# Optimization experiments

Measured on AMD Instinct MI355X. Metric: run time of the kernel, lower is better.

## Reference

```python
import jax, jax.numpy as jnp
import numpy as np

NUM_HEADS = 16
WINDOW = 16  # hard-coded in module; half-window = 8


def sliding_mask(seq_len):
    # mask[i, j] = 0 if j in [i - W//2, i + W//2], else -inf  (additive)
    i = jnp.arange(seq_len)[:, None]
    j = jnp.arange(seq_len)[None, :]
    return jnp.where(jnp.abs(i - j) <= WINDOW // 2, 0.0, -jnp.inf).astype(jnp.float32)


def setup_inputs() -> dict:
    key = jax.random.key(0)
    k1, k2, k3 = jax.random.split(key, 3)
    B, S, D = 2, 2048, 1024
    scale = 1.0 / np.sqrt(D)
    return {
        "input_embeddings": jax.random.normal(k1, (B, S, D), dtype=jnp.float32),
        "token_ids": jax.random.randint(k2, (B, S), 0, 32000, dtype=jnp.int64),
        # nn.MultiheadAttention params: packed in_proj [3D, D] + bias, out_proj [D, D] + bias
        "w_qkv": jax.random.normal(jax.random.fold_in(k3, 0), (3 * D, D), dtype=jnp.float32) * scale,
        "b_qkv": jnp.zeros((3 * D,), dtype=jnp.float32),
        "w_out": jax.random.normal(jax.random.fold_in(k3, 1), (D, D), dtype=jnp.float32) * scale,
        "b_out": jnp.zeros((D,), dtype=jnp.float32),
    }


def reference(input_embeddings, token_ids, w_qkv, b_qkv, w_out, b_out):
    B, S, D = input_embeddings.shape
    H = NUM_HEADS
    hd = D // H
    # packed QKV projection (torch in_proj): [B, S, 3D]
    qkv = input_embeddings @ w_qkv.T + b_qkv
    q, k, v = jnp.split(qkv, 3, axis=-1)
    # [B, H, S, hd]
    q = q.reshape(B, S, H, hd).transpose(0, 2, 1, 3)
    k = k.reshape(B, S, H, hd).transpose(0, 2, 1, 3)
    v = v.reshape(B, S, H, hd).transpose(0, 2, 1, 3)
    scores = jnp.einsum("bhqd,bhkd->bhqk", q, k) / jnp.sqrt(jnp.asarray(hd, q.dtype))
    scores = scores + sliding_mask(S)  # broadcast additive [S, S] mask
    attn = jax.nn.softmax(scores, axis=-1)
    ctx = jnp.einsum("bhqk,bhkd->bhqd", attn, v)
    ctx = ctx.transpose(0, 2, 1, 3).reshape(B, S, D)
    return ctx @ w_out.T + b_out
```

## Files before the change

kernel.cpp:

```cpp
#include <hip/hip_runtime.h>
#include <stdint.h>


typedef __bf16 bf16_t;
typedef bf16_t bf16x8 __attribute__((ext_vector_type(8)));
typedef unsigned short u16x8 __attribute__((ext_vector_type(8)));
typedef float f32x4 __attribute__((ext_vector_type(4)));

#define GLD16(g, l)                                                        \
  __builtin_amdgcn_global_load_lds(                                        \
      (const __attribute__((address_space(1))) void*)(g),                  \
      (__attribute__((address_space(3))) void*)(l), 16, 0, 0)

__device__ __forceinline__ unsigned short f2bf(float f) {
  unsigned int u = __float_as_uint(f);
  u += 0x7FFFu + ((u >> 16) & 1u);
  return (unsigned short)(u >> 16);
}

__device__ __forceinline__ bf16x8 ld16(const unsigned short* p) {
  return __builtin_bit_cast(bf16x8, *reinterpret_cast<const u16x8*>(p));
}

__global__ void cvt_all(const float* __restrict__ x, const float* __restrict__ wq,
                        const float* __restrict__ wo, unsigned short* __restrict__ xb,
                        unsigned short* __restrict__ wqb,
                        unsigned short* __restrict__ wob) {
  const int N0 = 1048576, N1 = 786432, N2 = 262144;
  for (int i = blockIdx.x * blockDim.x + threadIdx.x; i < N0 + N1 + N2;
       i += gridDim.x * blockDim.x) {
    const float4* src;
    unsigned short* dst;
    int j;
    if (i < N0) { src = (const float4*)x; dst = xb; j = i; }
    else if (i < N0 + N1) { src = (const float4*)wq; dst = wqb; j = i - N0; }
    else { src = (const float4*)wo; dst = wob; j = i - N0 - N1; }
    const float4 f = src[j];
    ushort4 o;
    o.x = f2bf(f.x); o.y = f2bf(f.y); o.z = f2bf(f.z); o.w = f2bf(f.w);
    reinterpret_cast<ushort4*>(dst)[j] = o;
  }
}

template <int EPI>
__global__ __launch_bounds__(256, 2) void gemm_bt(
    const unsigned short* __restrict__ A,
    const unsigned short* __restrict__ Bt,
    const float* __restrict__ bias,
    unsigned short* __restrict__ Cq, unsigned short* __restrict__ Ck,
    unsigned short* __restrict__ Cv, float* __restrict__ Cp, int M, int N,
    int K) {
  __shared__ unsigned short sA[2][8192];
  __shared__ unsigned short sB[2][8192];

  const int tid = threadIdx.x;
  const int wave = tid >> 6;
  const int lane = tid & 63;
  const int m0 = blockIdx.x * 128;
  const int n0 = blockIdx.y * 128;
  const int wr = wave >> 1;
  const int wc = wave & 1;

  f32x4 acc[4][4] = {};

  const int srow = (wave << 3) + (lane >> 3);
  const int sslot = ((lane & 7) ^ (lane >> 3)) << 3;
  const unsigned short* Ag = A + (size_t)(m0 + srow) * K + sslot;
  const unsigned short* Bg = Bt + (size_t)(n0 + srow) * K + sslot;
  const int wdst = wave * 512;

  const int T = K >> 6;

  auto stage = [&](int t, int b) {
#pragma unroll
    for (int r = 0; r < 4; ++r) {
      GLD16(Ag + (size_t)(r * 32) * K + t * 64, &sA[b][r * 2048 + wdst]);
      GLD16(Bg + (size_t)(r * 32) * K + t * 64, &sB[b][r * 2048 + wdst]);
    }
  };

  stage(0, 0);
  stage(1, 1);

  const int kg = lane >> 4;
  const int l7 = lane & 7;
  const int arr = wr * 64 + (lane & 15);
  const int brr = wc * 64 + (lane & 15);

  for (int t = 0; t < T; ++t) {
    if (t < T - 1)
      asm volatile("s_waitcnt vmcnt(8)" ::: "memory");
    else
      asm volatile("s_waitcnt vmcnt(0)" ::: "memory");
    __builtin_amdgcn_s_barrier();

    const int b = t & 1;
    const unsigned short* sAb = sA[b];
    const unsigned short* sBb = sB[b];
    bf16x8 af[2][4], bfr[2][4];
#pragma unroll
    for (int st = 0; st < 2; ++st) {
#pragma unroll
      for (int f = 0; f < 4; ++f) {
        const int se = ((st << 2) | kg) ^ l7;
        af[st][f] = ld16(&sAb[(arr + f * 16) * 64 + (se << 3)]);
        bfr[st][f] = ld16(&sBb[(brr + f * 16) * 64 + (se << 3)]);
      }
    }
    asm volatile("s_waitcnt lgkmcnt(0)" ::: "memory");
    __builtin_amdgcn_sched_barrier(0);
    __builtin_amdgcn_s_barrier();

    if (t + 2 < T) stage(t + 2, b);

#pragma unroll
    for (int st = 0; st < 2; ++st)
#pragma unroll
      for (int i = 0; i < 4; ++i)
#pragma unroll
        for (int j = 0; j < 4; ++j)
          acc[i][j] = __builtin_amdgcn_mfma_f32_16x16x32_bf16(
              af[st][i], bfr[st][j], acc[i][j], 0, 0, 0);
  }

#pragma unroll
  for (int i = 0; i < 4; ++i) {
    const int row0 = m0 + wr * 64 + i * 16 + ((lane >> 4) << 2);
#pragma unroll
    for (int j = 0; j < 4; ++j) {
      const int col = n0 + wc * 64 + j * 16 + (lane & 15);
      const float bb = bias[col];
#pragma unroll
      for (int r = 0; r < 4; ++r) {
        const int m = row0 + r;
        const float val = acc[i][j][r] + bb;
        if (EPI == 0) {
          Cp[(size_t)m * N + col] = val;
        } else {
          const int b2 = m >> 11, s = m & 2047;
          const int which = col >> 10, nn = col & 1023;
          const int h = nn >> 6, d = nn & 63;
          const int bh = (b2 << 4) + h;
          const unsigned short vb = f2bf(val);
          if (which == 0)
            Cq[((size_t)(bh * 2048 + s)) * 64 + d] = vb;
          else if (which == 1)
            Ck[((size_t)(bh * 2048 + s)) * 64 + d] = vb;
          else
            Cv[((size_t)(bh * 64 + d)) * 2048 + s] = vb;
        }
      }
    }
  }
}

__global__ __launch_bounds__(256) void attn_mfma(
    const unsigned short* __restrict__ Qb, const unsigned short* __restrict__ Kb,
    const unsigned short* __restrict__ Vt, unsigned short* __restrict__ ctx) {
  __shared__ unsigned short P[4][16][40];
  const int wave = threadIdx.x >> 6;
  const int lane = threadIdx.x & 63;
  const int gw = (blockIdx.x << 2) + wave;
  const int bh = gw >> 7;
  const int i0 = (gw & 127) << 4;
  const int qr = lane & 15;
  const int kg = lane >> 4;
  const int kc = kg << 3;

  const size_t qbase = ((size_t)(bh * 2048 + i0 + qr)) * 64;
  const bf16x8 aq0 = ld16(Qb + qbase + kc);
  const bf16x8 aq1 = ld16(Qb + qbase + 32 + kc);

  f32x4 sc0 = {0.f, 0.f, 0.f, 0.f}, sc1 = {0.f, 0.f, 0.f, 0.f};
  {
    const int ka0 = i0 - 8 + qr;
    const int ka1 = ka0 + 16;
    const int kcl0 = min(max(ka0, 0), 2047);
    const int kcl1 = min(max(ka1, 0), 2047);
    const unsigned short* K0 = Kb + ((size_t)(bh * 2048 + kcl0)) * 64;
    const unsigned short* K1 = Kb + ((size_t)(bh * 2048 + kcl1)) * 64;
    sc0 = __builtin_amdgcn_mfma_f32_16x16x32_bf16(aq0, ld16(K0 + kc), sc0, 0, 0, 0);
    sc0 = __builtin_amdgcn_mfma_f32_16x16x32_bf16(aq1, ld16(K0 + 32 + kc), sc0, 0, 0, 0);
    sc1 = __builtin_amdgcn_mfma_f32_16x16x32_bf16(aq0, ld16(K1 + kc), sc1, 0, 0, 0);
    sc1 = __builtin_amdgcn_mfma_f32_16x16x32_bf16(aq1, ld16(K1 + 32 + kc), sc1, 0, 0, 0);
  }

  unsigned short* Pw = &P[wave][0][0];
  float lsum[4];
#pragma unroll
  for (int r = 0; r < 4; ++r) {
    const int q = (kg << 2) + r;
    const int key0 = qr, key1 = 16 + qr;
    const int ka0 = i0 - 8 + key0, ka1 = i0 - 8 + key1;
    const bool v0 = (q <= key0) && (key0 <= q + 16) && (ka0 >= 0) && (ka0 < 2048);
    const bool v1 = (q <= key1) && (key1 <= q + 16) && (ka1 >= 0) && (ka1 < 2048);
    const float e0 = v0 ? __expf(sc0[r] * 0.125f) : 0.f;
    const float e1 = v1 ? __expf(sc1[r] * 0.125f) : 0.f;
    Pw[q * 40 + key0] = f2bf(e0);
    Pw[q * 40 + key1] = f2bf(e1);
    float s = e0 + e1;
#pragma unroll
    for (int off = 1; off < 16; off <<= 1) s += __shfl_xor(s, off);
    lsum[r] = s;
  }

  const bf16x8 pa = ld16(&Pw[qr * 40 + kc]);

  const int base_s = min(max(i0 - 8 + kc, 0), 2040);
  f32x4 o[4];
  const f32x4 zero = {0.f, 0.f, 0.f, 0.f};
#pragma unroll
  for (int t2 = 0; t2 < 4; ++t2) {
    const unsigned short* Vr =
        Vt + ((size_t)(bh * 64 + t2 * 16 + qr)) * 2048 + base_s;
    o[t2] = __builtin_amdgcn_mfma_f32_16x16x32_bf16(pa, ld16(Vr), zero, 0, 0, 0);
  }

  const int b = bh >> 4, h = bh & 15;
  float rinv[4];
#pragma unroll
  for (int r = 0; r < 4; ++r) rinv[r] = 1.0f / lsum[r];
#pragma unroll
  for (int t2 = 0; t2 < 4; ++t2) {
#pragma unroll
    for (int r = 0; r < 4; ++r) {
      const int q = (kg << 2) + r;
      const int d = t2 * 16 + qr;
      ctx[((size_t)(b * 2048 + i0 + q)) * 1024 + (h << 6) + d] =
          f2bf(o[t2][r] * rinv[r]);
    }
  }
}

extern "C" void kernel_launch(void* const* d_in, const int* in_sizes, int n_in,
                              void* d_out, int out_size, void* d_ws,
                              size_t ws_size, hipStream_t stream) {
  const float* x = (const float*)d_in[0];
  const float* w_qkv = (const float*)d_in[2];
  const float* b_qkv = (const float*)d_in[3];
  const float* w_out = (const float*)d_in[4];
  const float* b_out = (const float*)d_in[5];
  float* out = (float*)d_out;

  char* ws = (char*)d_ws;
  unsigned short* xb    = (unsigned short*)(ws + 0);
  unsigned short* wqkvb = (unsigned short*)(ws + 8388608);
  unsigned short* woutb = (unsigned short*)(ws + 14680064);
  unsigned short* Qb    = (unsigned short*)(ws + 16777216);
  unsigned short* Kb    = (unsigned short*)(ws + 25165824);
  unsigned short* Vt    = (unsigned short*)(ws + 33554432);
  unsigned short* ctxb  = (unsigned short*)(ws + 41943040);

  cvt_all<<<2048, 256, 0, stream>>>(x, w_qkv, w_out, xb, wqkvb, woutb);

  gemm_bt<1><<<dim3(32, 24), 256, 0, stream>>>(xb, wqkvb, b_qkv, Qb, Kb, Vt,
                                               nullptr, 4096, 3072, 1024);

  attn_mfma<<<1024, 256, 0, stream>>>(Qb, Kb, Vt, ctxb);

  gemm_bt<0><<<dim3(32, 8), 256, 0, stream>>>(ctxb, woutb, b_out, nullptr,
                                              nullptr, nullptr, out, 4096,
                                              1024, 1024);
}
```

Before: 79.73 us.

## Enlarge GEMM tiles to 256x256 with 512 threads and XCD-aware block remap

The GEMM kernel moves from 128x128 tiles with 256 threads to 256x256 tiles with 512 threads (8 waves in a 2x4 grid, each holding 8x4 MFMA accumulators). This raises arithmetic intensity per byte loaded into LDS. Block ids are remapped so consecutive ids are spread across the 8 XCDs, and the first k-half MFMAs are issued before the second half's LDS reads to overlap them. The risk is that the grid shrinks to 192 and 64 blocks, which may underfill the 256 CUs, especially for the output projection. Register pressure also rises.

```diff
diff --git a/kernel.cpp b/kernel.cpp
--- a/kernel.cpp
+++ b/kernel.cpp
@@ -43,25 +43,30 @@
 }
 
 template <int EPI>
-__global__ __launch_bounds__(256, 2) void gemm_bt(
+__global__ __launch_bounds__(512, 1) void gemm_bt(
     const unsigned short* __restrict__ A,
     const unsigned short* __restrict__ Bt,
     const float* __restrict__ bias,
     unsigned short* __restrict__ Cq, unsigned short* __restrict__ Ck,
     unsigned short* __restrict__ Cv, float* __restrict__ Cp, int M, int N,
-    int K) {
-  __shared__ unsigned short sA[2][8192];
-  __shared__ unsigned short sB[2][8192];
+    int K, int gny) {
+  __shared__ unsigned short sA[2][16384];
+  __shared__ unsigned short sB[2][16384];
 
   const int tid = threadIdx.x;
   const int wave = tid >> 6;
   const int lane = tid & 63;
-  const int m0 = blockIdx.x * 128;
-  const int n0 = blockIdx.y * 128;
-  const int wr = wave >> 1;
-  const int wc = wave & 1;
-
-  f32x4 acc[4][4] = {};
+
+  const int nwg = gridDim.x;
+  const int bid = blockIdx.x;
+  const int wg = (bid & 7) * (nwg >> 3) + (bid >> 3);
+  const int m0 = (wg / gny) * 256;
+  const int n0 = (wg % gny) * 256;
+
+  const int wr = wave >> 2;
+  const int wc = wave & 3;
+
+  f32x4 acc[8][4] = {};
 
   const int srow = (wave << 3) + (lane >> 3);
   const int sslot = ((lane & 7) ^ (lane >> 3)) << 3;
@@ -74,8 +79,8 @@
   auto stage = [&](int t, int b) {
 #pragma unroll
     for (int r = 0; r < 4; ++r) {
-      GLD16(Ag + (size_t)(r * 32) * K + t * 64, &sA[b][r * 2048 + wdst]);
-      GLD16(Bg + (size_t)(r * 32) * K + t * 64, &sB[b][r * 2048 + wdst]);
+      GLD16(Ag + (size_t)(r * 64) * K + t * 64, &sA[b][r * 4096 + wdst]);
+      GLD16(Bg + (size_t)(r * 64) * K + t * 64, &sB[b][r * 4096 + wdst]);
     }
   };
 
@@ -84,7 +89,7 @@
 
   const int kg = lane >> 4;
   const int l7 = lane & 7;
-  const int arr = wr * 64 + (lane & 15);
+  const int arr = wr * 128 + (lane & 15);
   const int brr = wc * 64 + (lane & 15);
 
   for (int t = 0; t < T; ++t) {
@@ -97,15 +102,27 @@
     const int b = t & 1;
     const unsigned short* sAb = sA[b];
     const unsigned short* sBb = sB[b];
-    bf16x8 af[2][4], bfr[2][4];
-#pragma unroll
-    for (int st = 0; st < 2; ++st) {
-#pragma unroll
-      for (int f = 0; f < 4; ++f) {
-        const int se = ((st << 2) | kg) ^ l7;
-        af[st][f] = ld16(&sAb[(arr + f * 16) * 64 + (se << 3)]);
-        bfr[st][f] = ld16(&sBb[(brr + f * 16) * 64 + (se << 3)]);
-      }
+
+    bf16x8 af0[8], bf0[4], af1[8], bf1[4];
+    {
+      const int se = kg ^ l7;
+#pragma unroll
+      for (int f = 0; f < 8; ++f) af0[f] = ld16(&sAb[(arr + f * 16) * 64 + (se << 3)]);
+#pragma unroll
+      for (int j = 0; j < 4; ++j) bf0[j] = ld16(&sBb[(brr + j * 16) * 64 + (se << 3)]);
+    }
+#pragma unroll
+    for (int i = 0; i < 8; ++i)
+#pragma unroll
+      for (int j = 0; j < 4; ++j)
+        acc[i][j] = __builtin_amdgcn_mfma_f32_16x16x32_bf16(af0[i], bf0[j],
+                                                            acc[i][j], 0, 0, 0);
+    {
+      const int se = (4 | kg) ^ l7;
+#pragma unroll
+      for (int f = 0; f < 8; ++f) af1[f] = ld16(&sAb[(arr + f * 16) * 64 + (se << 3)]);
+#pragma unroll
+      for (int j = 0; j < 4; ++j) bf1[j] = ld16(&sBb[(brr + j * 16) * 64 + (se << 3)]);
     }
     asm volatile("s_waitcnt lgkmcnt(0)" ::: "memory");
     __builtin_amdgcn_sched_barrier(0);
@@ -114,18 +131,16 @@
     if (t + 2 < T) stage(t + 2, b);
 
 #pragma unroll
-    for (int st = 0; st < 2; ++st)
-#pragma unroll
-      for (int i = 0; i < 4; ++i)
-#pragma unroll
-        for (int j = 0; j < 4; ++j)
-          acc[i][j] = __builtin_amdgcn_mfma_f32_16x16x32_bf16(
-              af[st][i], bfr[st][j], acc[i][j], 0, 0, 0);
-  }
-
-#pragma unroll
-  for (int i = 0; i < 4; ++i) {
-    const int row0 = m0 + wr * 64 + i * 16 + ((lane >> 4) << 2);
+    for (int i = 0; i < 8; ++i)
+#pragma unroll
+      for (int j = 0; j < 4; ++j)
+        acc[i][j] = __builtin_amdgcn_mfma_f32_16x16x32_bf16(af1[i], bf1[j],
+                                                            acc[i][j], 0, 0, 0);
+  }
+
+#pragma unroll
+  for (int i = 0; i < 8; ++i) {
+    const int row0 = m0 + wr * 128 + i * 16 + ((lane >> 4) << 2);
 #pragma unroll
     for (int j = 0; j < 4; ++j) {
       const int col = n0 + wc * 64 + j * 16 + (lane & 15);
@@ -253,12 +268,11 @@
 
   cvt_all<<<2048, 256, 0, stream>>>(x, w_qkv, w_out, xb, wqkvb, woutb);
 
-  gemm_bt<1><<<dim3(32, 24), 256, 0, stream>>>(xb, wqkvb, b_qkv, Qb, Kb, Vt,
-                                               nullptr, 4096, 3072, 1024);
+  gemm_bt<1><<<192, 512, 0, stream>>>(xb, wqkvb, b_qkv, Qb, Kb, Vt, nullptr,
+                                      4096, 3072, 1024, 12);
 
   attn_mfma<<<1024, 256, 0, stream>>>(Qb, Kb, Vt, ctxb);
 
-  gemm_bt<0><<<dim3(32, 8), 256, 0, stream>>>(ctxb, woutb, b_out, nullptr,
-                                              nullptr, nullptr, out, 4096,
-                                              1024, 1024);
-}
+  gemm_bt<0><<<64, 512, 0, stream>>>(ctxb, woutb, b_out, nullptr, nullptr,
+                                     nullptr, out, 4096, 1024, 1024, 4);
+}
```

Result: slower. 109.1 us (+36.8%).
